# Performance work log

Measured on AMD Instinct MI355X. Metric: run time of the kernel, lower is better.

## Reference

```python
import jax, jax.numpy as jnp
import numpy as np

N_NODES = 50000
N_EDGES = 800000
IN_DIM = 128
HID = 96
OUT_DIM = 128
N_LAYERS = 3


def setup_inputs() -> dict:
    key = jax.random.key(0)
    ks = jax.random.split(key, 10)
    x = jax.random.normal(ks[0], (N_NODES, IN_DIM), dtype=jnp.float32)
    edge_index = jax.random.randint(ks[1], (2, N_EDGES), 0, N_NODES, dtype=jnp.int32)
    s = 1.0 / np.sqrt(IN_DIM)
    W_in = jax.random.uniform(ks[2], (HID, IN_DIM), jnp.float32, -s, s)
    b_in = jax.random.uniform(ks[3], (HID,), jnp.float32, -s, s)
    sh = 1.0 / np.sqrt(HID)
    W_layers = jax.random.uniform(ks[4], (N_LAYERS, HID, HID), jnp.float32, -sh, sh)
    b_layers = jax.random.uniform(ks[5], (N_LAYERS, HID), jnp.float32, -sh, sh)
    sc = 1.0 / np.sqrt((N_LAYERS + 1) * HID)
    W_out = jax.random.uniform(ks[6], (OUT_DIM, (N_LAYERS + 1) * HID), jnp.float32, -sc, sc)
    b_out = jax.random.uniform(ks[7], (OUT_DIM,), jnp.float32, -sc, sc)
    return {"x": x, "edge_index": edge_index, "W_in": W_in, "b_in": b_in,
            "W_layers": W_layers, "b_layers": b_layers, "W_out": W_out, "b_out": b_out}


def reference(x, edge_index, W_in, b_in, W_layers, b_layers, W_out, b_out):
    src, dst = edge_index[0], edge_index[1]
    # input projection
    h = x @ W_in.T + b_in  # [N, HID]
    hidden_states = [h]
    for l in range(N_LAYERS):
        # GINConv (eps=0): nn((1+eps)*x_i + sum_{j in N(i)} x_j)
        agg = jax.ops.segment_sum(h[src], dst, num_segments=N_NODES)  # [N, HID]
        h = (h + agg) @ W_layers[l].T + b_layers[l]
        hidden_states.append(h)
    cat = jnp.concatenate(hidden_states, axis=1)  # [N, (L+1)*HID]
    return cat @ W_out.T + b_out
```

## Files before the change

### kernel.cpp

```cpp
#include <hip/hip_runtime.h>

#define NN   50000
#define NE   800000
#define IND  128
#define HIDD 96
#define OUTD 128
#define CATD (4 * HIDD)
#define CAP  64

typedef __attribute__((ext_vector_type(8))) short short8v;
typedef __attribute__((ext_vector_type(4))) float f32x4;

__device__ __forceinline__ ushort f2bf(float f) {
    unsigned u = __float_as_uint(f);
    u = (u + 0x7FFFu + ((u >> 16) & 1u)) >> 16;
    return (ushort)u;
}
__device__ __forceinline__ float bf2f(ushort h) {
    return __uint_as_float(((unsigned)h) << 16);
}

#define NW_IN  (HIDD * IND)
#define NW_L   (3 * HIDD * HIDD)
#define NW_OUT (OUTD * CATD)
#define NW_ROW (NW_IN + NW_L + NW_OUT)
#define NW_ALL (NW_ROW + NW_L + NW_OUT)

__global__ __launch_bounds__(256)
void wsplit_k(const float* __restrict__ Wi, const float* __restrict__ Wl,
              const float* __restrict__ Wo,
              ushort* __restrict__ whi, ushort* __restrict__ wlo)
{
    int i = blockIdx.x * 256 + threadIdx.x;
    if (i >= NW_ALL) return;
    float v;
    if (i < NW_ROW) {
        if (i < NW_IN)              v = Wi[i];
        else if (i < NW_IN + NW_L)  v = Wl[i - NW_IN];
        else                        v = Wo[i - NW_IN - NW_L];
    } else if (i < NW_ROW + NW_L) {
        int fi = i - NW_ROW;
        int l  = fi / 9216;
        int r  = fi - l * 9216;
        int c  = r / 1536;
        int ks = (r % 1536) / 512;
        int ln = (r % 512) / 8;
        int t  = r & 7;
        int j  = c * 16 + (ln & 15);
        int k  = ks * 32 + 8 * (ln >> 4) + t;
        v = Wl[(l * HIDD + j) * HIDD + k];
    } else {
        int fi = i - NW_ROW - NW_L;
        int c  = fi / 6144;
        int r  = fi - c * 6144;
        int ks = r / 512;
        int ln = (r % 512) / 8;
        int t  = r & 7;
        int j  = c * 16 + (ln & 15);
        int k  = ks * 32 + 8 * (ln >> 4) + t;
        v = Wo[j * CATD + k];
    }
    ushort h = f2bf(v);
    whi[i] = h;
    wlo[i] = f2bf(v - bf2f(h));
}

template<int K, int NCOLS, int ROWS, bool ACCUM>
__global__ __launch_bounds__(256)
void mgemm_k(const float* __restrict__ A,
             const ushort* __restrict__ Whi, const ushort* __restrict__ Wlo,
             int wstride, const float* __restrict__ bias,
             float* __restrict__ C, int cstride, int nrows)
{
    constexpr int ST  = K + 8;
    constexpr int KS  = K / 32;
    constexpr int NTR = ROWS / 16;
    constexpr int NTC = NCOLS / 16;
    constexpr int TRP = NTR / 2;
    constexpr int TCP = NTC / 2;
    constexpr int CPR = K / 8;

    __shared__ __align__(16) ushort sWh[NCOLS * ST];
    __shared__ __align__(16) ushort sWl[NCOLS * ST];

    const int tid  = threadIdx.x;
    const int w    = tid >> 6;
    const int l    = tid & 63;
    const int lr   = l & 15;
    const int lg   = l >> 4;
    const int row0 = blockIdx.x * ROWS;

    for (int idx = tid; idx < NCOLS * CPR; idx += 256) {
        int j = idx / CPR, c = idx - j * CPR;
        *(uint4*)&sWh[j * ST + c * 8] = *(const uint4*)&Whi[(long)j * wstride + c * 8];
        *(uint4*)&sWl[j * ST + c * 8] = *(const uint4*)&Wlo[(long)j * wstride + c * 8];
    }

    short8v Ah[TRP][KS], Al[TRP][KS];
#pragma unroll
    for (int i = 0; i < TRP; i++) {
        const int row = row0 + ((w >> 1) + 2 * i) * 16 + lr;
#pragma unroll
        for (int ks = 0; ks < KS; ks++) {
            float4 r0 = make_float4(0.f, 0.f, 0.f, 0.f);
            float4 r1 = make_float4(0.f, 0.f, 0.f, 0.f);
            if (row < nrows) {
                const float* p = &A[(long)row * K + ks * 32 + 8 * lg];
                r0 = *(const float4*)p;
                r1 = *(const float4*)(p + 4);
            }
            const float f[8] = {r0.x, r0.y, r0.z, r0.w, r1.x, r1.y, r1.z, r1.w};
            short8v hi, lo;
#pragma unroll
            for (int t = 0; t < 8; t++) {
                ushort h = f2bf(f[t]);
                hi[t] = (short)h;
                lo[t] = (short)f2bf(f[t] - bf2f(h));
            }
            Ah[i][ks] = hi;
            Al[i][ks] = lo;
        }
    }
    __syncthreads();

#pragma unroll
    for (int j = 0; j < TCP; j++) {
        const int colb = ((w & 1) + 2 * j) * 16;
        short8v Bh[KS], Bl[KS];
#pragma unroll
        for (int ks = 0; ks < KS; ks++) {
            Bh[ks] = *(const short8v*)&sWh[(colb + lr) * ST + ks * 32 + 8 * lg];
            Bl[ks] = *(const short8v*)&sWl[(colb + lr) * ST + ks * 32 + 8 * lg];
        }
        const float bv = bias ? bias[colb + lr] : 0.f;
#pragma unroll
        for (int i = 0; i < TRP; i++) {
            f32x4 acc = {bv, bv, bv, bv};
#pragma unroll
            for (int ks = 0; ks < KS; ks++) {
                acc = __builtin_amdgcn_mfma_f32_16x16x32_bf16(Ah[i][ks], Bh[ks], acc, 0, 0, 0);
                acc = __builtin_amdgcn_mfma_f32_16x16x32_bf16(Ah[i][ks], Bl[ks], acc, 0, 0, 0);
                acc = __builtin_amdgcn_mfma_f32_16x16x32_bf16(Al[i][ks], Bh[ks], acc, 0, 0, 0);
            }
#pragma unroll
            for (int p = 0; p < 4; p++) {
                const int row = row0 + ((w >> 1) + 2 * i) * 16 + 4 * lg + p;
                if (row < nrows) {
                    float* cp = &C[(long)row * cstride + colb + lr];
                    if (ACCUM) *cp += acc[p];
                    else       *cp  = acc[p];
                }
            }
        }
    }
}

__global__ __launch_bounds__(256)
void fillb_k(const int* __restrict__ ei, int* __restrict__ cursor,
             int* __restrict__ bucket)
{
    unsigned int e = blockIdx.x * 256u + threadIdx.x;
    if (e < (unsigned int)NE) {
        int s = ei[e];
        int d = ei[NE + e];
        int pos = atomicAdd(&cursor[d], 1);
        if (pos < CAP) bucket[(long)d * CAP + pos] = s;
    }
}

#define FROWS 32
#define FAST  100

__global__ __launch_bounds__(256)
void flayer_k(const float* __restrict__ h_in, int istride,
              const int* __restrict__ cursor, const int* __restrict__ bucket,
              const ushort* __restrict__ fWhi, const ushort* __restrict__ fWlo,
              const float* __restrict__ bias,
              float* __restrict__ h_out, int ostride)
{
    __shared__ __align__(16) float sA[FROWS * FAST];

    const int tid = threadIdx.x;
    const int n0  = blockIdx.x * FROWS;

    {
        const int i  = tid >> 3;
        const int st = tid & 7;
        const int n  = n0 + i;
        float4 s0 = make_float4(0.f, 0.f, 0.f, 0.f);
        float4 s1 = s0, s2 = s0;
        if (n < NN) {
            const float* hp = &h_in[(long)n * istride + st * 12];
            s0 = *(const float4*)hp;
            s1 = *(const float4*)(hp + 4);
            s2 = *(const float4*)(hp + 8);
            int cnt = cursor[n];
            if (cnt > CAP) cnt = CAP;
            const int* bp = &bucket[(long)n * CAP];
            int e = 0;
            for (; e + 1 < cnt; e += 2) {
                const float* q0 = &h_in[(long)bp[e]     * istride + st * 12];
                const float* q1 = &h_in[(long)bp[e + 1] * istride + st * 12];
                const float4 a0 = ((const float4*)q0)[0];
                const float4 b0 = *(const float4*)(q0 + 4);
                const float4 c0 = *(const float4*)(q0 + 8);
                const float4 a1 = ((const float4*)q1)[0];
                const float4 b1 = *(const float4*)(q1 + 4);
                const float4 c1 = *(const float4*)(q1 + 8);
                s0.x += a0.x + a1.x; s0.y += a0.y + a1.y; s0.z += a0.z + a1.z; s0.w += a0.w + a1.w;
                s1.x += b0.x + b1.x; s1.y += b0.y + b1.y; s1.z += b0.z + b1.z; s1.w += b0.w + b1.w;
                s2.x += c0.x + c1.x; s2.y += c0.y + c1.y; s2.z += c0.z + c1.z; s2.w += c0.w + c1.w;
            }
            if (e < cnt) {
                const float* q = &h_in[(long)bp[e] * istride + st * 12];
                const float4 a = ((const float4*)q)[0];
                const float4 b = *(const float4*)(q + 4);
                const float4 c = *(const float4*)(q + 8);
                s0.x += a.x; s0.y += a.y; s0.z += a.z; s0.w += a.w;
                s1.x += b.x; s1.y += b.y; s1.z += b.z; s1.w += b.w;
                s2.x += c.x; s2.y += c.y; s2.z += c.z; s2.w += c.w;
            }
        }
        float* ap = &sA[i * FAST + st * 12];
        ((float4*)ap)[0] = s0;
        ((float4*)ap)[1] = s1;
        ((float4*)ap)[2] = s2;
    }
    __syncthreads();

    const int w  = tid >> 6;
    const int l  = tid & 63;
    const int lr = l & 15;
    const int lg = l >> 4;
    const int tr = w >> 1;

    short8v Ah[3], Al[3];
#pragma unroll
    for (int ks = 0; ks < 3; ks++) {
        const float* ap = &sA[(tr * 16 + lr) * FAST + ks * 32 + 8 * lg];
        const float4 r0 = ((const float4*)ap)[0];
        const float4 r1 = ((const float4*)ap)[1];
        const float f[8] = {r0.x, r0.y, r0.z, r0.w, r1.x, r1.y, r1.z, r1.w};
        short8v hi, lo;
#pragma unroll
        for (int t = 0; t < 8; t++) {
            ushort h = f2bf(f[t]);
            hi[t] = (short)h;
            lo[t] = (short)f2bf(f[t] - bf2f(h));
        }
        Ah[ks] = hi;
        Al[ks] = lo;
    }

#pragma unroll
    for (int j = 0; j < 3; j++) {
        const int c    = (w & 1) + 2 * j;
        const int colb = c * 16;
        short8v Bh[3], Bl[3];
#pragma unroll
        for (int ks = 0; ks < 3; ks++) {
            Bh[ks] = *(const short8v*)&fWhi[((c * 3 + ks) * 64 + l) * 8];
            Bl[ks] = *(const short8v*)&fWlo[((c * 3 + ks) * 64 + l) * 8];
        }
        const float bv = bias[colb + lr];
        f32x4 acc = {bv, bv, bv, bv};
#pragma unroll
        for (int ks = 0; ks < 3; ks++) {
            acc = __builtin_amdgcn_mfma_f32_16x16x32_bf16(Ah[ks], Bh[ks], acc, 0, 0, 0);
            acc = __builtin_amdgcn_mfma_f32_16x16x32_bf16(Ah[ks], Bl[ks], acc, 0, 0, 0);
            acc = __builtin_amdgcn_mfma_f32_16x16x32_bf16(Al[ks], Bh[ks], acc, 0, 0, 0);
        }
#pragma unroll
        for (int p = 0; p < 4; p++) {
            const int row = n0 + tr * 16 + 4 * lg + p;
            if (row < NN)
                h_out[(long)row * ostride + colb + lr] = acc[p];
        }
    }
}

__global__ __launch_bounds__(256)
void fgemm_k(const float* __restrict__ cat, const ushort* __restrict__ fOhi,
             const ushort* __restrict__ fOlo, const float* __restrict__ bias,
             float* __restrict__ out)
{
    const int tid  = threadIdx.x;
    const int w    = tid >> 6;
    const int l    = tid & 63;
    const int lr   = l & 15;
    const int lg   = l >> 4;
    const int row0 = blockIdx.x * 64;

    f32x4 acc[2][4];
#pragma unroll
    for (int j = 0; j < 4; j++) {
        const float bv = bias[((w & 1) + 2 * j) * 16 + lr];
#pragma unroll
        for (int i = 0; i < 2; i++) acc[i][j] = (f32x4){bv, bv, bv, bv};
    }

#pragma unroll 4
    for (int ks = 0; ks < 12; ks++) {
        short8v Ah[2], Al[2];
#pragma unroll
        for (int i = 0; i < 2; i++) {
            const int row = row0 + ((w >> 1) + 2 * i) * 16 + lr;
            float4 r0 = make_float4(0.f, 0.f, 0.f, 0.f);
            float4 r1 = make_float4(0.f, 0.f, 0.f, 0.f);
            if (row < NN) {
                const float* p = &cat[(long)row * CATD + ks * 32 + 8 * lg];
                r0 = *(const float4*)p;
                r1 = *(const float4*)(p + 4);
            }
            const float f[8] = {r0.x, r0.y, r0.z, r0.w, r1.x, r1.y, r1.z, r1.w};
            short8v hi, lo;
#pragma unroll
            for (int t = 0; t < 8; t++) {
                ushort h = f2bf(f[t]);
                hi[t] = (short)h;
                lo[t] = (short)f2bf(f[t] - bf2f(h));
            }
            Ah[i] = hi;
            Al[i] = lo;
        }
#pragma unroll
        for (int j = 0; j < 4; j++) {
            const int c = (w & 1) + 2 * j;
            const short8v Bh = *(const short8v*)&fOhi[((c * 12 + ks) * 64 + l) * 8];
            const short8v Bl = *(const short8v*)&fOlo[((c * 12 + ks) * 64 + l) * 8];
#pragma unroll
            for (int i = 0; i < 2; i++) {
                acc[i][j] = __builtin_amdgcn_mfma_f32_16x16x32_bf16(Ah[i], Bh, acc[i][j], 0, 0, 0);
                acc[i][j] = __builtin_amdgcn_mfma_f32_16x16x32_bf16(Ah[i], Bl, acc[i][j], 0, 0, 0);
                acc[i][j] = __builtin_amdgcn_mfma_f32_16x16x32_bf16(Al[i], Bh, acc[i][j], 0, 0, 0);
            }
        }
    }

#pragma unroll
    for (int i = 0; i < 2; i++) {
#pragma unroll
        for (int p = 0; p < 4; p++) {
            const int row = row0 + ((w >> 1) + 2 * i) * 16 + 4 * lg + p;
            if (row < NN) {
#pragma unroll
                for (int j = 0; j < 4; j++)
                    out[(long)row * OUTD + ((w & 1) + 2 * j) * 16 + lr] = acc[i][j][p];
            }
        }
    }
}

extern "C" void kernel_launch(void* const* d_in, const int* in_sizes, int n_in,
                              void* d_out, int out_size, void* d_ws, size_t ws_size,
                              hipStream_t stream)
{
    const float* x  = (const float*)d_in[0];
    const int*   ei = (const int*)  d_in[1];
    const float* Wi = (const float*)d_in[2];
    const float* bi = (const float*)d_in[3];
    const float* Wl = (const float*)d_in[4];
    const float* bl = (const float*)d_in[5];
    const float* Wo = (const float*)d_in[6];
    const float* bo = (const float*)d_in[7];
    float* out = (float*)d_out;

    char* p = (char*)d_ws;
    int* cursor = (int*)p;                 p += ((size_t)NN * 4 + 255) & ~255ull;
    int* bucket = (int*)p;                 p += ((size_t)NN * CAP * 4 + 255) & ~255ull;
    ushort* whi = (ushort*)p;              p += ((size_t)NW_ALL * 2 + 255) & ~255ull;
    ushort* wlo = (ushort*)p;              p += ((size_t)NW_ALL * 2 + 255) & ~255ull;
    float* big  = (float*)p;
    const size_t used = (size_t)(p - (char*)d_ws);
    const bool catpath = (ws_size >= used + (size_t)NN * CATD * 4);

    const ushort* whi_in = whi;
    const ushort* wlo_in = wlo;
    const ushort* whi_o  = whi + NW_IN + NW_L;
    const ushort* wlo_o  = wlo + NW_IN + NW_L;
    const ushort* fLhi   = whi + NW_ROW;
    const ushort* fLlo   = wlo + NW_ROW;
    const ushort* fOhi   = whi + NW_ROW + NW_L;
    const ushort* fOlo   = wlo + NW_ROW + NW_L;

    hipLaunchKernelGGL(wsplit_k, dim3((NW_ALL + 255) / 256), dim3(256), 0, stream,
                       Wi, Wl, Wo, whi, wlo);
    hipMemsetAsync(cursor, 0, (size_t)NN * sizeof(int), stream);
    hipLaunchKernelGGL(fillb_k, dim3((NE + 255) / 256), dim3(256), 0, stream,
                       ei, cursor, bucket);

    if (catpath) {
        float* cat = big;
        hipLaunchKernelGGL((mgemm_k<IND, HIDD, 32, false>),
                           dim3((NN + 31) / 32), dim3(256), 0, stream,
                           x, whi_in, wlo_in, IND, bi, cat, CATD, NN);
        for (int l = 0; l < 3; l++) {
            hipLaunchKernelGGL(flayer_k, dim3((NN + FROWS - 1) / FROWS), dim3(256), 0, stream,
                               cat + (size_t)l * HIDD, CATD, cursor, bucket,
                               fLhi + (size_t)l * 9216, fLlo + (size_t)l * 9216,
                               bl + (size_t)l * HIDD,
                               cat + (size_t)(l + 1) * HIDD, CATD);
        }
        hipLaunchKernelGGL(fgemm_k, dim3((NN + 63) / 64), dim3(256), 0, stream,
                           cat, fOhi, fOlo, bo, out);
    } else {
        float* hA = big;
        float* hB = hA + (size_t)NN * HIDD;
        hipLaunchKernelGGL((mgemm_k<IND, HIDD, 32, false>),
                           dim3((NN + 31) / 32), dim3(256), 0, stream,
                           x, whi_in, wlo_in, IND, bi, hA, HIDD, NN);
        hipLaunchKernelGGL((mgemm_k<HIDD, OUTD, 64, false>),
                           dim3((NN + 63) / 64), dim3(256), 0, stream,
                           hA, whi_o, wlo_o, CATD, bo, out, OUTD, NN);
        const float* hsrc = hA;
        float*       hdst = hB;
        for (int l = 0; l < 3; l++) {
            hipLaunchKernelGGL(flayer_k, dim3((NN + FROWS - 1) / FROWS), dim3(256), 0, stream,
                               hsrc, HIDD, cursor, bucket,
                               fLhi + (size_t)l * 9216, fLlo + (size_t)l * 9216,
                               bl + (size_t)l * HIDD, hdst, HIDD);
            hipLaunchKernelGGL((mgemm_k<HIDD, OUTD, 64, true>),
                               dim3((NN + 63) / 64), dim3(256), 0, stream,
                               hdst, whi_o + (size_t)(l + 1) * HIDD,
                               wlo_o + (size_t)(l + 1) * HIDD, CATD,
                               (const float*)nullptr, out, OUTD, NN);
            const float* t = hsrc; hsrc = hdst; hdst = (float*)t;
        }
    }
}
```

Before: 361.1 us.

## Pad neighbor buckets to multiples of four with a zero sentinel row for 4-wide gathers

Bucket lists are padded to a multiple of four using a sentinel node index that points at an added zero row, so the aggregation loop can load four neighbor indices as an int4 and issue four row gathers per iteration with no tail handling. This aims to raise memory-level parallelism in the gather. Bucket fill now handles four edges per thread with vectorized index loads. The layer kernel is cut to 16 rows and 128 threads per block to give more blocks. The cost is an extra padding kernel, extra memsets for the sentinel row, and gathers of zero rows for padded slots.

```diff
diff --git a/kernel.cpp b/kernel.cpp
--- a/kernel.cpp
+++ b/kernel.cpp
@@ -74,10 +74,8 @@
 {
     constexpr int ST  = K + 8;
     constexpr int KS  = K / 32;
-    constexpr int NTR = ROWS / 16;
-    constexpr int NTC = NCOLS / 16;
-    constexpr int TRP = NTR / 2;
-    constexpr int TCP = NTC / 2;
+    constexpr int TRP = (ROWS / 16) / 2;
+    constexpr int TCP = (NCOLS / 16) / 2;
     constexpr int CPR = K / 8;
 
     __shared__ __align__(16) ushort sWh[NCOLS * ST];
@@ -159,19 +157,44 @@
 void fillb_k(const int* __restrict__ ei, int* __restrict__ cursor,
              int* __restrict__ bucket)
 {
-    unsigned int e = blockIdx.x * 256u + threadIdx.x;
-    if (e < (unsigned int)NE) {
-        int s = ei[e];
-        int d = ei[NE + e];
-        int pos = atomicAdd(&cursor[d], 1);
-        if (pos < CAP) bucket[(long)d * CAP + pos] = s;
-    }
-}
-
-#define FROWS 32
+    unsigned int e0 = (blockIdx.x * 256u + threadIdx.x) * 4u;
+    if (e0 + 4 <= (unsigned int)NE) {
+        const int4 s4 = *(const int4*)&ei[e0];
+        const int4 d4 = *(const int4*)&ei[NE + e0];
+        int p0 = atomicAdd(&cursor[d4.x], 1);
+        int p1 = atomicAdd(&cursor[d4.y], 1);
+        int p2 = atomicAdd(&cursor[d4.z], 1);
+        int p3 = atomicAdd(&cursor[d4.w], 1);
+        if (p0 < CAP) bucket[(long)d4.x * CAP + p0] = s4.x;
+        if (p1 < CAP) bucket[(long)d4.y * CAP + p1] = s4.y;
+        if (p2 < CAP) bucket[(long)d4.z * CAP + p2] = s4.z;
+        if (p3 < CAP) bucket[(long)d4.w * CAP + p3] = s4.w;
+    } else {
+        for (unsigned int e = e0; e < (unsigned int)NE; e++) {
+            int s = ei[e];
+            int d = ei[NE + e];
+            int pos = atomicAdd(&cursor[d], 1);
+            if (pos < CAP) bucket[(long)d * CAP + pos] = s;
+        }
+    }
+}
+
+__global__ __launch_bounds__(256)
+void padb_k(const int* __restrict__ cursor, int* __restrict__ bucket)
+{
+    int n = blockIdx.x * 256 + threadIdx.x;
+    if (n >= NN) return;
+    int cnt = cursor[n];
+    if (cnt > CAP) cnt = CAP;
+    int cnt4 = (cnt + 3) & ~3;
+    int* bp = &bucket[(long)n * CAP];
+    for (int p = cnt; p < cnt4; p++) bp[p] = NN;
+}
+
+#define FROWS 16
 #define FAST  100
 
-__global__ __launch_bounds__(256)
+__global__ __launch_bounds__(128)
 void flayer_k(const float* __restrict__ h_in, int istride,
               const int* __restrict__ cursor, const int* __restrict__ bucket,
               const ushort* __restrict__ fWhi, const ushort* __restrict__ fWlo,
@@ -187,39 +210,48 @@
         const int i  = tid >> 3;
         const int st = tid & 7;
         const int n  = n0 + i;
-        float4 s0 = make_float4(0.f, 0.f, 0.f, 0.f);
-        float4 s1 = s0, s2 = s0;
-        if (n < NN) {
-            const float* hp = &h_in[(long)n * istride + st * 12];
-            s0 = *(const float4*)hp;
+        const float* hbase = h_in + st * 12;
+        float4 s0, s1, s2;
+        {
+            const float* hp = &hbase[(long)n * istride];
+            s0 = ((const float4*)hp)[0];
             s1 = *(const float4*)(hp + 4);
             s2 = *(const float4*)(hp + 8);
-            int cnt = cursor[n];
-            if (cnt > CAP) cnt = CAP;
-            const int* bp = &bucket[(long)n * CAP];
-            int e = 0;
-            for (; e + 1 < cnt; e += 2) {
-                const float* q0 = &h_in[(long)bp[e]     * istride + st * 12];
-                const float* q1 = &h_in[(long)bp[e + 1] * istride + st * 12];
-                const float4 a0 = ((const float4*)q0)[0];
-                const float4 b0 = *(const float4*)(q0 + 4);
-                const float4 c0 = *(const float4*)(q0 + 8);
-                const float4 a1 = ((const float4*)q1)[0];
-                const float4 b1 = *(const float4*)(q1 + 4);
-                const float4 c1 = *(const float4*)(q1 + 8);
-                s0.x += a0.x + a1.x; s0.y += a0.y + a1.y; s0.z += a0.z + a1.z; s0.w += a0.w + a1.w;
-                s1.x += b0.x + b1.x; s1.y += b0.y + b1.y; s1.z += b0.z + b1.z; s1.w += b0.w + b1.w;
-                s2.x += c0.x + c1.x; s2.y += c0.y + c1.y; s2.z += c0.z + c1.z; s2.w += c0.w + c1.w;
-            }
-            if (e < cnt) {
-                const float* q = &h_in[(long)bp[e] * istride + st * 12];
-                const float4 a = ((const float4*)q)[0];
-                const float4 b = *(const float4*)(q + 4);
-                const float4 c = *(const float4*)(q + 8);
-                s0.x += a.x; s0.y += a.y; s0.z += a.z; s0.w += a.w;
-                s1.x += b.x; s1.y += b.y; s1.z += b.z; s1.w += b.w;
-                s2.x += c.x; s2.y += c.y; s2.z += c.z; s2.w += c.w;
-            }
+        }
+        int cnt = cursor[n];
+        if (cnt > CAP) cnt = CAP;
+        const int cnt4 = (cnt + 3) & ~3;
+        const int* bp = &bucket[(long)n * CAP];
+        for (int e = 0; e < cnt4; e += 4) {
+            const int4 id = *(const int4*)&bp[e];
+            const float* q0 = &hbase[(long)id.x * istride];
+            const float* q1 = &hbase[(long)id.y * istride];
+            const float* q2 = &hbase[(long)id.z * istride];
+            const float* q3 = &hbase[(long)id.w * istride];
+            const float4 a0 = ((const float4*)q0)[0];
+            const float4 b0 = *(const float4*)(q0 + 4);
+            const float4 c0 = *(const float4*)(q0 + 8);
+            const float4 a1 = ((const float4*)q1)[0];
+            const float4 b1 = *(const float4*)(q1 + 4);
+            const float4 c1 = *(const float4*)(q1 + 8);
+            const float4 a2 = ((const float4*)q2)[0];
+            const float4 b2 = *(const float4*)(q2 + 4);
+            const float4 c2 = *(const float4*)(q2 + 8);
+            const float4 a3 = ((const float4*)q3)[0];
+            const float4 b3 = *(const float4*)(q3 + 4);
+            const float4 c3 = *(const float4*)(q3 + 8);
+            s0.x += (a0.x + a1.x) + (a2.x + a3.x);
+            s0.y += (a0.y + a1.y) + (a2.y + a3.y);
+            s0.z += (a0.z + a1.z) + (a2.z + a3.z);
+            s0.w += (a0.w + a1.w) + (a2.w + a3.w);
+            s1.x += (b0.x + b1.x) + (b2.x + b3.x);
+            s1.y += (b0.y + b1.y) + (b2.y + b3.y);
+            s1.z += (b0.z + b1.z) + (b2.z + b3.z);
+            s1.w += (b0.w + b1.w) + (b2.w + b3.w);
+            s2.x += (c0.x + c1.x) + (c2.x + c3.x);
+            s2.y += (c0.y + c1.y) + (c2.y + c3.y);
+            s2.z += (c0.z + c1.z) + (c2.z + c3.z);
+            s2.w += (c0.w + c1.w) + (c2.w + c3.w);
         }
         float* ap = &sA[i * FAST + st * 12];
         ((float4*)ap)[0] = s0;
@@ -232,12 +264,11 @@
     const int l  = tid & 63;
     const int lr = l & 15;
     const int lg = l >> 4;
-    const int tr = w >> 1;
 
     short8v Ah[3], Al[3];
 #pragma unroll
     for (int ks = 0; ks < 3; ks++) {
-        const float* ap = &sA[(tr * 16 + lr) * FAST + ks * 32 + 8 * lg];
+        const float* ap = &sA[lr * FAST + ks * 32 + 8 * lg];
         const float4 r0 = ((const float4*)ap)[0];
         const float4 r1 = ((const float4*)ap)[1];
         const float f[8] = {r0.x, r0.y, r0.z, r0.w, r1.x, r1.y, r1.z, r1.w};
@@ -254,7 +285,7 @@
 
 #pragma unroll
     for (int j = 0; j < 3; j++) {
-        const int c    = (w & 1) + 2 * j;
+        const int c    = w + 2 * j;
         const int colb = c * 16;
         short8v Bh[3], Bl[3];
 #pragma unroll
@@ -272,7 +303,7 @@
         }
 #pragma unroll
         for (int p = 0; p < 4; p++) {
-            const int row = n0 + tr * 16 + 4 * lg + p;
+            const int row = n0 + 4 * lg + p;
             if (row < NN)
                 h_out[(long)row * ostride + colb + lr] = acc[p];
         }
@@ -372,7 +403,7 @@
     ushort* wlo = (ushort*)p;              p += ((size_t)NW_ALL * 2 + 255) & ~255ull;
     float* big  = (float*)p;
     const size_t used = (size_t)(p - (char*)d_ws);
-    const bool catpath = (ws_size >= used + (size_t)NN * CATD * 4);
+    const bool catpath = (ws_size >= used + (size_t)(NN + 1) * CATD * 4);
 
     const ushort* whi_in = whi;
     const ushort* wlo_in = wlo;
@@ -386,16 +417,19 @@
     hipLaunchKernelGGL(wsplit_k, dim3((NW_ALL + 255) / 256), dim3(256), 0, stream,
                        Wi, Wl, Wo, whi, wlo);
     hipMemsetAsync(cursor, 0, (size_t)NN * sizeof(int), stream);
-    hipLaunchKernelGGL(fillb_k, dim3((NE + 255) / 256), dim3(256), 0, stream,
+    hipLaunchKernelGGL(fillb_k, dim3((NE / 4 + 255) / 256), dim3(256), 0, stream,
                        ei, cursor, bucket);
+    hipLaunchKernelGGL(padb_k, dim3((NN + 255) / 256), dim3(256), 0, stream,
+                       cursor, bucket);
 
     if (catpath) {
         float* cat = big;
+        hipMemsetAsync(cat + (size_t)NN * CATD, 0, CATD * sizeof(float), stream);
         hipLaunchKernelGGL((mgemm_k<IND, HIDD, 32, false>),
                            dim3((NN + 31) / 32), dim3(256), 0, stream,
                            x, whi_in, wlo_in, IND, bi, cat, CATD, NN);
         for (int l = 0; l < 3; l++) {
-            hipLaunchKernelGGL(flayer_k, dim3((NN + FROWS - 1) / FROWS), dim3(256), 0, stream,
+            hipLaunchKernelGGL(flayer_k, dim3((NN + FROWS - 1) / FROWS), dim3(128), 0, stream,
                                cat + (size_t)l * HIDD, CATD, cursor, bucket,
                                fLhi + (size_t)l * 9216, fLlo + (size_t)l * 9216,
                                bl + (size_t)l * HIDD,
@@ -405,7 +439,9 @@
                            cat, fOhi, fOlo, bo, out);
     } else {
         float* hA = big;
-        float* hB = hA + (size_t)NN * HIDD;
+        float* hB = hA + (size_t)(NN + 1) * HIDD;
+        hipMemsetAsync(hA + (size_t)NN * HIDD, 0, HIDD * sizeof(float), stream);
+        hipMemsetAsync(hB + (size_t)NN * HIDD, 0, HIDD * sizeof(float), stream);
         hipLaunchKernelGGL((mgemm_k<IND, HIDD, 32, false>),
                            dim3((NN + 31) / 32), dim3(256), 0, stream,
                            x, whi_in, wlo_in, IND, bi, hA, HIDD, NN);
@@ -415,7 +451,7 @@
         const float* hsrc = hA;
         float*       hdst = hB;
         for (int l = 0; l < 3; l++) {
-            hipLaunchKernelGGL(flayer_k, dim3((NN + FROWS - 1) / FROWS), dim3(256), 0, stream,
+            hipLaunchKernelGGL(flayer_k, dim3((NN + FROWS - 1) / FROWS), dim3(128), 0, stream,
                                hsrc, HIDD, cursor, bucket,
                                fLhi + (size_t)l * 9216, fLlo + (size_t)l * 9216,
                                bl + (size_t)l * HIDD, hdst, HIDD);
```

New measurement: 393.8 us. 1.09x slower.

## Gather neighbor features from bf16 copies and vectorize edge bucketing

Applied to the files above, without the earlier changes.

Each layer now writes a bf16 shadow copy of its output, and the neighbor aggregation gathers 16-bit features instead of fp32. This halves the bytes moved in the random gather, which dominates each GIN layer, but drops the neighbor terms to bf16 precision. It also adds a conversion kernel for the input-projection output and extra stores per layer. The edge-bucketing kernel is changed to load four edges per thread with int4 loads.

```diff
diff --git a/kernel.cpp b/kernel.cpp
--- a/kernel.cpp
+++ b/kernel.cpp
@@ -19,6 +19,8 @@
 __device__ __forceinline__ float bf2f(ushort h) {
     return __uint_as_float(((unsigned)h) << 16);
 }
+__device__ __forceinline__ float blo(unsigned u) { return __uint_as_float(u << 16); }
+__device__ __forceinline__ float bhi(unsigned u) { return __uint_as_float(u & 0xffff0000u); }
 
 #define NW_IN  (HIDD * IND)
 #define NW_L   (3 * HIDD * HIDD)
@@ -74,10 +76,8 @@
 {
     constexpr int ST  = K + 8;
     constexpr int KS  = K / 32;
-    constexpr int NTR = ROWS / 16;
-    constexpr int NTC = NCOLS / 16;
-    constexpr int TRP = NTR / 2;
-    constexpr int TCP = NTC / 2;
+    constexpr int TRP = (ROWS / 16) / 2;
+    constexpr int TCP = (NCOLS / 16) / 2;
     constexpr int CPR = K / 8;
 
     __shared__ __align__(16) ushort sWh[NCOLS * ST];
@@ -159,24 +159,57 @@
 void fillb_k(const int* __restrict__ ei, int* __restrict__ cursor,
              int* __restrict__ bucket)
 {
-    unsigned int e = blockIdx.x * 256u + threadIdx.x;
-    if (e < (unsigned int)NE) {
-        int s = ei[e];
-        int d = ei[NE + e];
-        int pos = atomicAdd(&cursor[d], 1);
-        if (pos < CAP) bucket[(long)d * CAP + pos] = s;
-    }
+    unsigned int e0 = (blockIdx.x * 256u + threadIdx.x) * 4u;
+    if (e0 + 4 <= (unsigned int)NE) {
+        const int4 s4 = *(const int4*)&ei[e0];
+        const int4 d4 = *(const int4*)&ei[NE + e0];
+        int p0 = atomicAdd(&cursor[d4.x], 1);
+        int p1 = atomicAdd(&cursor[d4.y], 1);
+        int p2 = atomicAdd(&cursor[d4.z], 1);
+        int p3 = atomicAdd(&cursor[d4.w], 1);
+        if (p0 < CAP) bucket[(long)d4.x * CAP + p0] = s4.x;
+        if (p1 < CAP) bucket[(long)d4.y * CAP + p1] = s4.y;
+        if (p2 < CAP) bucket[(long)d4.z * CAP + p2] = s4.z;
+        if (p3 < CAP) bucket[(long)d4.w * CAP + p3] = s4.w;
+    } else {
+        for (unsigned int e = e0; e < (unsigned int)NE; e++) {
+            int s = ei[e];
+            int d = ei[NE + e];
+            int pos = atomicAdd(&cursor[d], 1);
+            if (pos < CAP) bucket[(long)d * CAP + pos] = s;
+        }
+    }
+}
+
+__global__ __launch_bounds__(256)
+void hcvt_k(const float* __restrict__ hf, int istride, ushort* __restrict__ hb)
+{
+    int idx = blockIdx.x * 256 + threadIdx.x;
+    if (idx >= NN * (HIDD / 8)) return;
+    int row = idx / (HIDD / 8);
+    int c   = (idx - row * (HIDD / 8)) * 8;
+    const float* p = &hf[(long)row * istride + c];
+    const float4 r0 = *(const float4*)p;
+    const float4 r1 = *(const float4*)(p + 4);
+    uint4 o;
+    o.x = (unsigned)f2bf(r0.x) | ((unsigned)f2bf(r0.y) << 16);
+    o.y = (unsigned)f2bf(r0.z) | ((unsigned)f2bf(r0.w) << 16);
+    o.z = (unsigned)f2bf(r1.x) | ((unsigned)f2bf(r1.y) << 16);
+    o.w = (unsigned)f2bf(r1.z) | ((unsigned)f2bf(r1.w) << 16);
+    *(uint4*)&hb[(long)row * HIDD + c] = o;
 }
 
 #define FROWS 32
 #define FAST  100
 
 __global__ __launch_bounds__(256)
-void flayer_k(const float* __restrict__ h_in, int istride,
+void flayer_k(const float* __restrict__ hf_in, int istride,
+              const ushort* __restrict__ hb_in,
               const int* __restrict__ cursor, const int* __restrict__ bucket,
               const ushort* __restrict__ fWhi, const ushort* __restrict__ fWlo,
               const float* __restrict__ bias,
-              float* __restrict__ h_out, int ostride)
+              float* __restrict__ hf_out, int ostride,
+              ushort* __restrict__ hb_out)
 {
     __shared__ __align__(16) float sA[FROWS * FAST];
 
@@ -190,36 +223,33 @@
         float4 s0 = make_float4(0.f, 0.f, 0.f, 0.f);
         float4 s1 = s0, s2 = s0;
         if (n < NN) {
-            const float* hp = &h_in[(long)n * istride + st * 12];
-            s0 = *(const float4*)hp;
+            const float* hp = &hf_in[(long)n * istride + st * 12];
+            s0 = ((const float4*)hp)[0];
             s1 = *(const float4*)(hp + 4);
             s2 = *(const float4*)(hp + 8);
             int cnt = cursor[n];
             if (cnt > CAP) cnt = CAP;
             const int* bp = &bucket[(long)n * CAP];
+            const ushort* hbb = hb_in + st * 12;
+#define ACCB(q)                                                              \
+            { const uint2 a = *(const uint2*)(q);                            \
+              const uint2 b = *(const uint2*)((q) + 4);                      \
+              const uint2 c = *(const uint2*)((q) + 8);                      \
+              s0.x += blo(a.x); s0.y += bhi(a.x); s0.z += blo(a.y); s0.w += bhi(a.y); \
+              s1.x += blo(b.x); s1.y += bhi(b.x); s1.z += blo(b.y); s1.w += bhi(b.y); \
+              s2.x += blo(c.x); s2.y += bhi(c.x); s2.z += blo(c.y); s2.w += bhi(c.y); }
             int e = 0;
             for (; e + 1 < cnt; e += 2) {
-                const float* q0 = &h_in[(long)bp[e]     * istride + st * 12];
-                const float* q1 = &h_in[(long)bp[e + 1] * istride + st * 12];
-                const float4 a0 = ((const float4*)q0)[0];
-                const float4 b0 = *(const float4*)(q0 + 4);
-                const float4 c0 = *(const float4*)(q0 + 8);
-                const float4 a1 = ((const float4*)q1)[0];
-                const float4 b1 = *(const float4*)(q1 + 4);
-                const float4 c1 = *(const float4*)(q1 + 8);
-                s0.x += a0.x + a1.x; s0.y += a0.y + a1.y; s0.z += a0.z + a1.z; s0.w += a0.w + a1.w;
-                s1.x += b0.x + b1.x; s1.y += b0.y + b1.y; s1.z += b0.z + b1.z; s1.w += b0.w + b1.w;
-                s2.x += c0.x + c1.x; s2.y += c0.y + c1.y; s2.z += c0.z + c1.z; s2.w += c0.w + c1.w;
+                const int2 id = *(const int2*)&bp[e];
+                const ushort* q0 = &hbb[(long)id.x * HIDD];
+                const ushort* q1 = &hbb[(long)id.y * HIDD];
+                ACCB(q0); ACCB(q1);
             }
             if (e < cnt) {
-                const float* q = &h_in[(long)bp[e] * istride + st * 12];
-                const float4 a = ((const float4*)q)[0];
-                const float4 b = *(const float4*)(q + 4);
-                const float4 c = *(const float4*)(q + 8);
-                s0.x += a.x; s0.y += a.y; s0.z += a.z; s0.w += a.w;
-                s1.x += b.x; s1.y += b.y; s1.z += b.z; s1.w += b.w;
-                s2.x += c.x; s2.y += c.y; s2.z += c.z; s2.w += c.w;
-            }
+                const ushort* q = &hbb[(long)bp[e] * HIDD];
+                ACCB(q);
+            }
+#undef ACCB
         }
         float* ap = &sA[i * FAST + st * 12];
         ((float4*)ap)[0] = s0;
@@ -273,8 +303,11 @@
 #pragma unroll
         for (int p = 0; p < 4; p++) {
             const int row = n0 + tr * 16 + 4 * lg + p;
-            if (row < NN)
-                h_out[(long)row * ostride + colb + lr] = acc[p];
+            if (row < NN) {
+                hf_out[(long)row * ostride + colb + lr] = acc[p];
+                if (hb_out)
+                    hb_out[(long)row * HIDD + colb + lr] = f2bf(acc[p]);
+            }
         }
     }
 }
@@ -370,6 +403,8 @@
     int* bucket = (int*)p;                 p += ((size_t)NN * CAP * 4 + 255) & ~255ull;
     ushort* whi = (ushort*)p;              p += ((size_t)NW_ALL * 2 + 255) & ~255ull;
     ushort* wlo = (ushort*)p;              p += ((size_t)NW_ALL * 2 + 255) & ~255ull;
+    ushort* hbfA = (ushort*)p;             p += ((size_t)NN * HIDD * 2 + 255) & ~255ull;
+    ushort* hbfB = (ushort*)p;             p += ((size_t)NN * HIDD * 2 + 255) & ~255ull;
     float* big  = (float*)p;
     const size_t used = (size_t)(p - (char*)d_ws);
     const bool catpath = (ws_size >= used + (size_t)NN * CATD * 4);
@@ -386,7 +421,7 @@
     hipLaunchKernelGGL(wsplit_k, dim3((NW_ALL + 255) / 256), dim3(256), 0, stream,
                        Wi, Wl, Wo, whi, wlo);
     hipMemsetAsync(cursor, 0, (size_t)NN * sizeof(int), stream);
-    hipLaunchKernelGGL(fillb_k, dim3((NE + 255) / 256), dim3(256), 0, stream,
+    hipLaunchKernelGGL(fillb_k, dim3((NE / 4 + 255) / 256), dim3(256), 0, stream,
                        ei, cursor, bucket);
 
     if (catpath) {
@@ -394,13 +429,19 @@
         hipLaunchKernelGGL((mgemm_k<IND, HIDD, 32, false>),
                            dim3((NN + 31) / 32), dim3(256), 0, stream,
                            x, whi_in, wlo_in, IND, bi, cat, CATD, NN);
-        for (int l = 0; l < 3; l++) {
-            hipLaunchKernelGGL(flayer_k, dim3((NN + FROWS - 1) / FROWS), dim3(256), 0, stream,
-                               cat + (size_t)l * HIDD, CATD, cursor, bucket,
-                               fLhi + (size_t)l * 9216, fLlo + (size_t)l * 9216,
-                               bl + (size_t)l * HIDD,
-                               cat + (size_t)(l + 1) * HIDD, CATD);
-        }
+        hipLaunchKernelGGL(hcvt_k, dim3((NN * (HIDD / 8) + 255) / 256), dim3(256), 0, stream,
+                           cat, CATD, hbfA);
+        hipLaunchKernelGGL(flayer_k, dim3((NN + FROWS - 1) / FROWS), dim3(256), 0, stream,
+                           cat, CATD, hbfA, cursor, bucket,
+                           fLhi, fLlo, bl, cat + HIDD, CATD, hbfB);
+        hipLaunchKernelGGL(flayer_k, dim3((NN + FROWS - 1) / FROWS), dim3(256), 0, stream,
+                           cat + HIDD, CATD, hbfB, cursor, bucket,
+                           fLhi + 9216, fLlo + 9216, bl + HIDD,
+                           cat + 2 * HIDD, CATD, hbfA);
+        hipLaunchKernelGGL(flayer_k, dim3((NN + FROWS - 1) / FROWS), dim3(256), 0, stream,
+                           cat + 2 * HIDD, CATD, hbfA, cursor, bucket,
+                           fLhi + 2 * 9216, fLlo + 2 * 9216, bl + 2 * HIDD,
+                           cat + 3 * HIDD, CATD, (ushort*)nullptr);
         hipLaunchKernelGGL(fgemm_k, dim3((NN + 63) / 64), dim3(256), 0, stream,
                            cat, fOhi, fOlo, bo, out);
     } else {
@@ -412,19 +453,23 @@
         hipLaunchKernelGGL((mgemm_k<HIDD, OUTD, 64, false>),
                            dim3((NN + 63) / 64), dim3(256), 0, stream,
                            hA, whi_o, wlo_o, CATD, bo, out, OUTD, NN);
-        const float* hsrc = hA;
-        float*       hdst = hB;
+        hipLaunchKernelGGL(hcvt_k, dim3((NN * (HIDD / 8) + 255) / 256), dim3(256), 0, stream,
+                           hA, HIDD, hbfA);
+        const float* hsrc = hA;  float* hdst = hB;
+        ushort* bsrc = hbfA;     ushort* bdst = hbfB;
         for (int l = 0; l < 3; l++) {
             hipLaunchKernelGGL(flayer_k, dim3((NN + FROWS - 1) / FROWS), dim3(256), 0, stream,
-                               hsrc, HIDD, cursor, bucket,
+                               hsrc, HIDD, bsrc, cursor, bucket,
                                fLhi + (size_t)l * 9216, fLlo + (size_t)l * 9216,
-                               bl + (size_t)l * HIDD, hdst, HIDD);
+                               bl + (size_t)l * HIDD, hdst, HIDD,
+                               (l < 2) ? bdst : (ushort*)nullptr);
             hipLaunchKernelGGL((mgemm_k<HIDD, OUTD, 64, true>),
                                dim3((NN + 63) / 64), dim3(256), 0, stream,
                                hdst, whi_o + (size_t)(l + 1) * HIDD,
                                wlo_o + (size_t)(l + 1) * HIDD, CATD,
                                (const float*)nullptr, out, OUTD, NN);
             const float* t = hsrc; hsrc = hdst; hdst = (float*)t;
-        }
-    }
-}
+            ushort* tb = bsrc; bsrc = bdst; bdst = tb;
+        }
+    }
+}
```

Result: faster. 329.8 us (-8.7%).
